# Kernel optimization log

Measured on AMD Instinct MI355X. Metric: run time of the kernel, lower is better.

The kernel has to match this reference:

```python
import jax, jax.numpy as jnp
import numpy as np
from jax import lax

V = 5          # IMU nodes
C = 128        # channels
T = 128        # timesteps
B = 128        # batch
K = 3          # st_kernel_size (non-causal)
V_TH = 0.8     # LIF threshold
TAU = 2.0      # LIF default tau (spikingjelly)
EPS = 1e-5


def setup_inputs() -> dict:
    key = jax.random.key(0)
    ks = jax.random.split(key, 6)
    # binary spike input [T, B, C, 2V]
    x_spike = (jax.random.uniform(ks[0], (T, B, C, 2 * V)) < 0.5).astype(jnp.float32)
    # modality fusion conv1d: [C, 2C, 1], kaiming-ish scale
    W_fusion = jax.random.normal(ks[1], (C, 2 * C, 1), jnp.float32) * (1.0 / np.sqrt(2 * C))
    gn1_w = jnp.ones((C,), jnp.float32)
    gn1_b = jnp.zeros((C,), jnp.float32)
    # node mixer conv1d over time: [V, V, K]
    W_mixer = jax.random.normal(ks[2], (V, V, K), jnp.float32) * (1.0 / np.sqrt(V * K))
    gn2_w = jnp.ones((V,), jnp.float32)
    gn2_b = jnp.zeros((V,), jnp.float32)
    # learnable adjacency: eye + 0.01*randn
    adj = jnp.eye(V, dtype=jnp.float32) + 0.01 * jax.random.normal(ks[3], (V, V), jnp.float32)
    return {"x_spike": x_spike, "W_fusion": W_fusion, "gn1_w": gn1_w, "gn1_b": gn1_b,
            "W_mixer": W_mixer, "gn2_w": gn2_w, "gn2_b": gn2_b, "adj": adj}


def groupnorm1(x, w, b):
    # single-group GroupNorm on [N, C, L]: normalize over (C, L) per sample
    mu = jnp.mean(x, axis=(1, 2), keepdims=True)
    var = jnp.var(x, axis=(1, 2), keepdims=True)
    xn = (x - mu) * lax.rsqrt(var + EPS)
    return xn * w[None, :, None] + b[None, :, None]


def lif_multistep(x_seq):
    # spikingjelly LIFNode, step_mode='m', decay_input=True, hard reset to 0
    def step(v, x):
        v = v + (x - v) / TAU
        s = (v >= V_TH).astype(x.dtype)
        v = v * (1.0 - s)
        return v, s
    _, spikes = lax.scan(step, jnp.zeros_like(x_seq[0]), x_seq)
    return spikes


def reference(x_spike, W_fusion, gn1_w, gn1_b, W_mixer, gn2_w, gn2_b, adj):
    Tn, Bn, Cn, N = x_spike.shape
    # ---- dual-modality fusion ----
    acc, gyr = x_spike[..., :V], x_spike[..., V:]
    fused = jnp.concatenate([acc, gyr], axis=2).reshape(Tn * Bn, 2 * Cn, V)  # [TB, 2C, V]
    y = jnp.einsum('oc,ncv->nov', W_fusion[:, :, 0], fused)                   # 1x1 conv
    y = groupnorm1(y, gn1_w, gn1_b)
    x_nodes = lif_multistep(y.reshape(Tn, Bn, Cn, V))                         # [T,B,C,V]
    # ---- adaptive topology temporal conv ----
    x_bt = x_nodes.transpose(1, 2, 3, 0).reshape(Bn * Cn, V, Tn)              # [BC, V, T]
    pad = K // 2
    x_bt = jnp.pad(x_bt, ((0, 0), (0, 0), (pad, pad)))
    sym = 0.5 * (adj + adj.T)
    masked_w = W_mixer * jax.nn.sigmoid(sym)[:, :, None]                      # [V, V, K]
    y_bt = lax.conv_general_dilated(x_bt, masked_w, (1,), 'VALID',
                                    dimension_numbers=('NCH', 'OIH', 'NCH'))
    y_bt = y_bt[..., :Tn]
    y_bt = groupnorm1(y_bt, gn2_w, gn2_b)
    y_mixed = y_bt.reshape(Bn, Cn, V, Tn).transpose(3, 0, 1, 2)               # [T,B,C,V]
    out = lif_multistep(y_mixed)
    return jnp.concatenate([out, out], axis=-1)                               # [T,B,C,2V]
```

## Files before the change

kernel.cpp:

```cpp
#include <hip/hip_runtime.h>
#include <cstdint>
#include <cstddef>

#define NV 5
#define NC 128
#define NT 128
#define NB 128
typedef unsigned long long ull;

__device__ __forceinline__ float fa(float a, float b){ return __fadd_rn(a,b); }
__device__ __forceinline__ float fm(float a, float b){ return __fmul_rn(a,b); }
__device__ __forceinline__ float fs(float a, float b){ return __fsub_rn(a,b); }

__device__ __forceinline__ float base80(const float* a)
{
    float r0=a[0],r1=a[1],r2=a[2],r3=a[3],r4=a[4],r5=a[5],r6=a[6],r7=a[7];
    #pragma unroll
    for (int i = 8; i < 80; i += 8) {
        r0=fa(r0,a[i+0]); r1=fa(r1,a[i+1]); r2=fa(r2,a[i+2]); r3=fa(r3,a[i+3]);
        r4=fa(r4,a[i+4]); r5=fa(r5,a[i+5]); r6=fa(r6,a[i+6]); r7=fa(r7,a[i+7]);
    }
    return fa(fa(fa(r0,r1),fa(r2,r3)), fa(fa(r4,r5),fa(r6,r7)));
}

__device__ __forceinline__ float base80v(const float* a, float mu)
{
    float r[8];
    #pragma unroll
    for (int j = 0; j < 8; ++j) { const float d = fs(a[j], mu); r[j] = fm(d, d); }
    #pragma unroll
    for (int i = 8; i < 80; i += 8)
        #pragma unroll
        for (int j = 0; j < 8; ++j) {
            const float d = fs(a[i + j], mu);
            r[j] = fa(r[j], fm(d, d));
        }
    return fa(fa(fa(r[0],r[1]),fa(r[2],r[3])), fa(fa(r[4],r[5]),fa(r[6],r[7])));
}

__global__ __launch_bounds__(256) void kT(const float* __restrict__ W,
                                          float* __restrict__ Wt)
{
    const int i = blockIdx.x * 256 + threadIdx.x;
    const int c = i >> 7, o = i & 127;
    Wt[i] = W[o * 256 + c];
}

__global__ __launch_bounds__(128) void kA(const float* __restrict__ x,
                                          const float* __restrict__ Wt,
                                          const float* __restrict__ g1w,
                                          const float* __restrict__ g1b,
                                          float* __restrict__ y1)
{
    const int n0 = blockIdx.x * 4;
    const int o  = threadIdx.x;

    __shared__ float xs_raw[4 * 256 * 8];
    __shared__ float statA[4][4];
    __shared__ float muS[4], rstdS[4];
    float (*xs)[256][8] = (float (*)[256][8])xs_raw;

    {
        const float4* xg = (const float4*)(x + (size_t)n0 * 1280);
        #pragma unroll
        for (int it = 0; it < 10; ++it) {
            const int q = it * 128 + o;
            const float4 val = xg[q];
            const int f = q * 4;
            const int g = f >> 10 >> 0 ? f / 1280 : 0;
            const int gg = f / 1280;
            int r = f - gg * 1280;
            float tmp[4] = {val.x, val.y, val.z, val.w};
            #pragma unroll
            for (int e = 0; e < 4; ++e) {
                const int c = r / 10, j = r - c * 10;
                const int fc = (j < 5) ? c : c + 128;
                const int v  = (j < 5) ? j : j - 5;
                xs[gg][fc][v] = tmp[e];
                ++r;
            }
            (void)g;
        }
    }
    __syncthreads();

    float acc[4][NV];
    #pragma unroll
    for (int g = 0; g < 4; ++g)
        #pragma unroll
        for (int v = 0; v < NV; ++v) acc[g][v] = 0.f;

    #pragma unroll 4
    for (int fc = 0; fc < 256; ++fc) {
        const float A = Wt[fc * 128 + o];
        #pragma unroll
        for (int g = 0; g < 4; ++g) {
            const float4 xv = *(const float4*)&xs[g][fc][0];
            const float  x4 = xs[g][fc][4];
            acc[g][0] = fa(acc[g][0], fm(A, xv.x));
            acc[g][1] = fa(acc[g][1], fm(A, xv.y));
            acc[g][2] = fa(acc[g][2], fm(A, xv.z));
            acc[g][3] = fa(acc[g][3], fm(A, xv.w));
            acc[g][4] = fa(acc[g][4], fm(A, x4));
        }
    }
    __syncthreads();

    float* ys = xs_raw;
    float* dsv = xs_raw + 2560;

    #pragma unroll
    for (int g = 0; g < 4; ++g)
        #pragma unroll
        for (int v = 0; v < NV; ++v) ys[g * 640 + o * 5 + v] = acc[g][v];
    __syncthreads();

    if (threadIdx.x < 16) {
        const int g = threadIdx.x >> 2, p = threadIdx.x & 3;
        const float b0 = base80(&ys[g * 640 + (2 * p) * 80]);
        const float b1 = base80(&ys[g * 640 + (2 * p + 1) * 80]);
        statA[g][p] = fa(b0, b1);
    }
    __syncthreads();
    if (threadIdx.x < 4) {
        const int g = threadIdx.x;
        const float tot = fa(fa(statA[g][0], statA[g][1]), fa(statA[g][2], statA[g][3]));
        muS[g] = __fdiv_rn(tot, 640.f);
    }
    __syncthreads();

    #pragma unroll
    for (int g = 0; g < 4; ++g) {
        const float mu = muS[g];
        #pragma unroll
        for (int v = 0; v < NV; ++v) {
            const float d = fs(acc[g][v], mu);
            dsv[g * 640 + o * 5 + v] = fm(d, d);
        }
    }
    __syncthreads();
    if (threadIdx.x < 16) {
        const int g = threadIdx.x >> 2, p = threadIdx.x & 3;
        const float b0 = base80(&dsv[g * 640 + (2 * p) * 80]);
        const float b1 = base80(&dsv[g * 640 + (2 * p + 1) * 80]);
        statA[g][p] = fa(b0, b1);
    }
    __syncthreads();
    if (threadIdx.x < 4) {
        const int g = threadIdx.x;
        const float tot = fa(fa(statA[g][0], statA[g][1]), fa(statA[g][2], statA[g][3]));
        const float var = __fdiv_rn(tot, 640.f);
        rstdS[g] = __fdiv_rn(1.f, __fsqrt_rn(fa(var, 1e-5f)));
    }
    __syncthreads();

    const float wf = g1w[o], bf = g1b[o];
    #pragma unroll
    for (int g = 0; g < 4; ++g) {
        const float mu = muS[g], rstd = rstdS[g];
        const int n = n0 + g;
        #pragma unroll
        for (int v = 0; v < NV; ++v) {
            const float xn = fm(fs(acc[g][v], mu), rstd);
            y1[(size_t)n * 640 + o * 5 + v] = fa(fm(xn, wf), bf);
        }
    }
}

__global__ __launch_bounds__(320) void kB1(const float* __restrict__ y1,
                                           ulonglong2* __restrict__ masks)
{
    const int b   = blockIdx.x >> 1;
    const int c0  = (blockIdx.x & 1) * 64;
    const int tid = threadIdx.x;

    ull lo = 0ull, hi = 0ull;
    float vm = 0.f;
    const float* p = y1 + (size_t)b * 640 + (size_t)c0 * 5 + tid;
    for (int t0 = 0; t0 < NT; t0 += 16) {
        float xv[16];
        #pragma unroll
        for (int j = 0; j < 16; ++j)
            xv[j] = p[(size_t)(t0 + j) * (NB * 640)];
        #pragma unroll
        for (int j = 0; j < 16; ++j) {
            vm = fa(vm, fm(fs(xv[j], vm), 0.5f));
            if (vm >= 0.8f) {
                const int t = t0 + j;
                if (t < 64) lo |= 1ull << t; else hi |= 1ull << (t - 64);
                vm = 0.f;
            }
        }
    }
    masks[(size_t)b * 640 + (size_t)c0 * 5 + tid] = make_ulonglong2(lo, hi);
}

__device__ __forceinline__ float bitf(ull lo, ull hi, int t)
{
    if (t < 0 || t > 127) return 0.f;
    return (float)(((t < 64) ? (lo >> t) : (hi >> (t - 64))) & 1ull);
}

__global__ __launch_bounds__(512) void kB2(const ulonglong2* __restrict__ masks,
                                           const float* __restrict__ Wm,
                                           const float* __restrict__ g2w,
                                           const float* __restrict__ g2b,
                                           const float* __restrict__ adj,
                                           float* __restrict__ out)
{
    const int blk = blockIdx.x;
    const int b   = blk >> 5;
    const int c0  = (blk & 31) * 4;
    const int tid = threadIdx.x;
    const int p   = tid >> 7;
    const int lt  = tid & 127;

    __shared__ float mw_s[75];
    __shared__ ull   m_lo[4][5], m_hi[4][5];
    __shared__ float conv_s[4][5][128];
    __shared__ float spk_s[128][40];
    __shared__ float stat_s[4][8];
    __shared__ float mu_s[4], rstd_s[4];

    if (tid < 75) {
        const int oo = tid / 15, rem = tid % 15, ii = rem / 3;
        const float sym = fm(0.5f, fa(adj[oo * 5 + ii], adj[ii * 5 + oo]));
        const float e = (float)exp(-(double)sym);
        const float sig = __fdiv_rn(1.f, fa(1.f, e));
        mw_s[tid] = fm(Wm[tid], sig);
    }
    if (tid < 20) {
        const int pp = tid / 5, vv = tid % 5;
        const ulonglong2 m = masks[((size_t)b * 128 + c0 + pp) * 5 + vv];
        m_lo[pp][vv] = m.x; m_hi[pp][vv] = m.y;
    }
    __syncthreads();

    {
        float bv[5][3];
        #pragma unroll
        for (int i = 0; i < 5; ++i) {
            const ull lo = m_lo[p][i], hi = m_hi[p][i];
            #pragma unroll
            for (int k = 0; k < 3; ++k)
                bv[i][k] = bitf(lo, hi, lt - 1 + k);
        }
        #pragma unroll
        for (int o = 0; o < 5; ++o) {
            float res = 0.f;
            #pragma unroll
            for (int i = 0; i < 5; ++i)
                #pragma unroll
                for (int k = 0; k < 3; ++k)
                    res = fa(res, fm(mw_s[(o * 5 + i) * 3 + k], bv[i][k]));
            conv_s[p][o][lt] = res;
        }
    }
    __syncthreads();

    if (lt < 8)
        stat_s[p][lt] = base80(&conv_s[p][0][0] + lt * 80);
    __syncthreads();
    if (lt == 0) {
        const float* s = stat_s[p];
        const float tot = fa(fa(fa(s[0],s[1]),fa(s[2],s[3])),
                             fa(fa(s[4],s[5]),fa(s[6],s[7])));
        mu_s[p] = __fdiv_rn(tot, 640.f);
    }
    __syncthreads();

    if (lt < 8)
        stat_s[p][lt] = base80v(&conv_s[p][0][0] + lt * 80, mu_s[p]);
    __syncthreads();
    if (lt == 0) {
        const float* s = stat_s[p];
        const float tot = fa(fa(fa(s[0],s[1]),fa(s[2],s[3])),
                             fa(fa(s[4],s[5]),fa(s[6],s[7])));
        const float var = __fdiv_rn(tot, 640.f);
        rstd_s[p] = __fdiv_rn(1.f, __fsqrt_rn(fa(var, 1e-5f)));
    }
    __syncthreads();

    if (lt < 5) {
        const int o = lt;
        const float mu = mu_s[p], rstd = rstd_s[p];
        const float gw = g2w[o], gb = g2b[o];
        float vm = 0.f;
        for (int t = 0; t < NT; ++t) {
            const float z  = conv_s[p][o][t];
            const float xn = fm(fs(z, mu), rstd);
            const float yn = fa(fm(xn, gw), gb);
            vm = fa(vm, fm(fs(yn, vm), 0.5f));
            const bool sp = (vm >= 0.8f);
            if (sp) vm = 0.f;
            const float so = sp ? 1.f : 0.f;
            spk_s[t][p * 10 + o]     = so;
            spk_s[t][p * 10 + 5 + o] = so;
        }
    }
    __syncthreads();

    for (int q = tid; q < 1280; q += 512) {
        const int t = q / 10, s = q - t * 10;
        float4* dst = (float4*)(out + ((size_t)(t * NB + b) * 1280 + c0 * 10));
        dst[s] = reinterpret_cast<const float4*>(&spk_s[t][0])[s];
    }
}

extern "C" void kernel_launch(void* const* d_in, const int* in_sizes, int n_in,
                              void* d_out, int out_size, void* d_ws, size_t ws_size,
                              hipStream_t stream)
{
    const float* x   = (const float*)d_in[0];
    const float* W   = (const float*)d_in[1];
    const float* g1w = (const float*)d_in[2];
    const float* g1b = (const float*)d_in[3];
    const float* Wm  = (const float*)d_in[4];
    const float* g2w = (const float*)d_in[5];
    const float* g2b = (const float*)d_in[6];
    const float* adj = (const float*)d_in[7];
    float* out = (float*)d_out;

    float* y1 = (float*)d_ws;
    ulonglong2* masks = (ulonglong2*)((char*)d_ws + (64u << 20));
    float* Wt = (float*)((char*)d_ws + (80u << 20));

    hipLaunchKernelGGL(kT, dim3(128), dim3(256), 0, stream, W, Wt);
    hipLaunchKernelGGL(kA, dim3(NT * NB / 4), dim3(128), 0, stream,
                       x, Wt, g1w, g1b, y1);
    hipLaunchKernelGGL(kB1, dim3(NB * 2), dim3(320), 0, stream,
                       y1, masks);
    hipLaunchKernelGGL(kB2, dim3(4096), dim3(512), 0, stream,
                       masks, Wm, g2w, g2b, adj, out);
}
```

Baseline: 201.7 us.

## Compute two output channels per thread in fusion GEMM with packed smem layout

The fusion kernel now runs 64 threads per block, each computing two output channels, so every shared-memory input value read is reused for two weight columns. The staged input is repacked as [fc][g*5+v] with 20 contiguous floats per input channel, so one fc row loads as five float4s instead of strided per-group reads. This cuts LDS traffic per FMA. In exchange it doubles accumulator registers and halves the threads per block, which may reduce latency hiding and add load-loop iterations.

```diff
diff --git a/kernel.cpp b/kernel.cpp
--- a/kernel.cpp
+++ b/kernel.cpp
@@ -46,123 +46,141 @@
     Wt[i] = W[o * 256 + c];
 }
 
-__global__ __launch_bounds__(128) void kA(const float* __restrict__ x,
-                                          const float* __restrict__ Wt,
-                                          const float* __restrict__ g1w,
-                                          const float* __restrict__ g1b,
-                                          float* __restrict__ y1)
+__global__ __launch_bounds__(64) void kA(const float* __restrict__ x,
+                                         const float* __restrict__ Wt,
+                                         const float* __restrict__ g1w,
+                                         const float* __restrict__ g1b,
+                                         float* __restrict__ y1)
 {
     const int n0 = blockIdx.x * 4;
-    const int o  = threadIdx.x;
-
-    __shared__ float xs_raw[4 * 256 * 8];
+    const int t  = threadIdx.x;
+
+    __shared__ __align__(16) float xs[256 * 20];
     __shared__ float statA[4][4];
     __shared__ float muS[4], rstdS[4];
-    float (*xs)[256][8] = (float (*)[256][8])xs_raw;
 
     {
         const float4* xg = (const float4*)(x + (size_t)n0 * 1280);
         #pragma unroll
-        for (int it = 0; it < 10; ++it) {
-            const int q = it * 128 + o;
+        for (int it = 0; it < 20; ++it) {
+            const int q = it * 64 + t;
             const float4 val = xg[q];
-            const int f = q * 4;
-            const int g = f >> 10 >> 0 ? f / 1280 : 0;
-            const int gg = f / 1280;
-            int r = f - gg * 1280;
             float tmp[4] = {val.x, val.y, val.z, val.w};
-            #pragma unroll
-            for (int e = 0; e < 4; ++e) {
-                const int c = r / 10, j = r - c * 10;
+            int r = q * 4;
+            #pragma unroll
+            for (int e = 0; e < 4; ++e, ++r) {
+                const int g  = r / 1280;
+                const int rr = r - g * 1280;
+                const int c  = rr / 10;
+                const int j  = rr - c * 10;
                 const int fc = (j < 5) ? c : c + 128;
                 const int v  = (j < 5) ? j : j - 5;
-                xs[gg][fc][v] = tmp[e];
-                ++r;
-            }
-            (void)g;
-        }
-    }
-    __syncthreads();
-
-    float acc[4][NV];
-    #pragma unroll
-    for (int g = 0; g < 4; ++g)
-        #pragma unroll
-        for (int v = 0; v < NV; ++v) acc[g][v] = 0.f;
-
-    #pragma unroll 4
+                xs[fc * 20 + g * 5 + v] = tmp[e];
+            }
+        }
+    }
+    __syncthreads();
+
+    float acc[2][4][NV];
+    #pragma unroll
+    for (int oi = 0; oi < 2; ++oi)
+        #pragma unroll
+        for (int g = 0; g < 4; ++g)
+            #pragma unroll
+            for (int v = 0; v < NV; ++v) acc[oi][g][v] = 0.f;
+
+    #pragma unroll 2
     for (int fc = 0; fc < 256; ++fc) {
-        const float A = Wt[fc * 128 + o];
-        #pragma unroll
-        for (int g = 0; g < 4; ++g) {
-            const float4 xv = *(const float4*)&xs[g][fc][0];
-            const float  x4 = xs[g][fc][4];
-            acc[g][0] = fa(acc[g][0], fm(A, xv.x));
-            acc[g][1] = fa(acc[g][1], fm(A, xv.y));
-            acc[g][2] = fa(acc[g][2], fm(A, xv.z));
-            acc[g][3] = fa(acc[g][3], fm(A, xv.w));
-            acc[g][4] = fa(acc[g][4], fm(A, x4));
-        }
-    }
-    __syncthreads();
-
-    float* ys = xs_raw;
-    float* dsv = xs_raw + 2560;
-
-    #pragma unroll
-    for (int g = 0; g < 4; ++g)
-        #pragma unroll
-        for (int v = 0; v < NV; ++v) ys[g * 640 + o * 5 + v] = acc[g][v];
-    __syncthreads();
-
-    if (threadIdx.x < 16) {
-        const int g = threadIdx.x >> 2, p = threadIdx.x & 3;
+        const float A0 = Wt[fc * 128 + t];
+        const float A1 = Wt[fc * 128 + 64 + t];
+        const float4 q0 = *(const float4*)&xs[fc * 20 + 0];
+        const float4 q1 = *(const float4*)&xs[fc * 20 + 4];
+        const float4 q2 = *(const float4*)&xs[fc * 20 + 8];
+        const float4 q3 = *(const float4*)&xs[fc * 20 + 12];
+        const float4 q4 = *(const float4*)&xs[fc * 20 + 16];
+        const float xv[20] = {q0.x,q0.y,q0.z,q0.w, q1.x,q1.y,q1.z,q1.w,
+                              q2.x,q2.y,q2.z,q2.w, q3.x,q3.y,q3.z,q3.w,
+                              q4.x,q4.y,q4.z,q4.w};
+        #pragma unroll
+        for (int g = 0; g < 4; ++g)
+            #pragma unroll
+            for (int v = 0; v < NV; ++v) {
+                acc[0][g][v] = fa(acc[0][g][v], fm(A0, xv[g * 5 + v]));
+                acc[1][g][v] = fa(acc[1][g][v], fm(A1, xv[g * 5 + v]));
+            }
+    }
+    __syncthreads();
+
+    float* ys  = xs;
+    float* dsv = xs + 2560;
+
+    #pragma unroll
+    for (int oi = 0; oi < 2; ++oi) {
+        const int o = t + oi * 64;
+        #pragma unroll
+        for (int g = 0; g < 4; ++g)
+            #pragma unroll
+            for (int v = 0; v < NV; ++v)
+                ys[g * 640 + o * 5 + v] = acc[oi][g][v];
+    }
+    __syncthreads();
+
+    if (t < 16) {
+        const int g = t >> 2, p = t & 3;
         const float b0 = base80(&ys[g * 640 + (2 * p) * 80]);
         const float b1 = base80(&ys[g * 640 + (2 * p + 1) * 80]);
         statA[g][p] = fa(b0, b1);
     }
     __syncthreads();
-    if (threadIdx.x < 4) {
-        const int g = threadIdx.x;
+    if (t < 4) {
+        const int g = t;
         const float tot = fa(fa(statA[g][0], statA[g][1]), fa(statA[g][2], statA[g][3]));
         muS[g] = __fdiv_rn(tot, 640.f);
     }
     __syncthreads();
 
     #pragma unroll
-    for (int g = 0; g < 4; ++g) {
-        const float mu = muS[g];
-        #pragma unroll
-        for (int v = 0; v < NV; ++v) {
-            const float d = fs(acc[g][v], mu);
-            dsv[g * 640 + o * 5 + v] = fm(d, d);
-        }
-    }
-    __syncthreads();
-    if (threadIdx.x < 16) {
-        const int g = threadIdx.x >> 2, p = threadIdx.x & 3;
+    for (int oi = 0; oi < 2; ++oi) {
+        const int o = t + oi * 64;
+        #pragma unroll
+        for (int g = 0; g < 4; ++g) {
+            const float mu = muS[g];
+            #pragma unroll
+            for (int v = 0; v < NV; ++v) {
+                const float d = fs(acc[oi][g][v], mu);
+                dsv[g * 640 + o * 5 + v] = fm(d, d);
+            }
+        }
+    }
+    __syncthreads();
+    if (t < 16) {
+        const int g = t >> 2, p = t & 3;
         const float b0 = base80(&dsv[g * 640 + (2 * p) * 80]);
         const float b1 = base80(&dsv[g * 640 + (2 * p + 1) * 80]);
         statA[g][p] = fa(b0, b1);
     }
     __syncthreads();
-    if (threadIdx.x < 4) {
-        const int g = threadIdx.x;
+    if (t < 4) {
+        const int g = t;
         const float tot = fa(fa(statA[g][0], statA[g][1]), fa(statA[g][2], statA[g][3]));
         const float var = __fdiv_rn(tot, 640.f);
         rstdS[g] = __fdiv_rn(1.f, __fsqrt_rn(fa(var, 1e-5f)));
     }
     __syncthreads();
 
-    const float wf = g1w[o], bf = g1b[o];
-    #pragma unroll
-    for (int g = 0; g < 4; ++g) {
-        const float mu = muS[g], rstd = rstdS[g];
-        const int n = n0 + g;
-        #pragma unroll
-        for (int v = 0; v < NV; ++v) {
-            const float xn = fm(fs(acc[g][v], mu), rstd);
-            y1[(size_t)n * 640 + o * 5 + v] = fa(fm(xn, wf), bf);
+    #pragma unroll
+    for (int oi = 0; oi < 2; ++oi) {
+        const int o = t + oi * 64;
+        const float wf = g1w[o], bf = g1b[o];
+        #pragma unroll
+        for (int g = 0; g < 4; ++g) {
+            const float mu = muS[g], rstd = rstdS[g];
+            const int n = n0 + g;
+            #pragma unroll
+            for (int v = 0; v < NV; ++v) {
+                const float xn = fm(fs(acc[oi][g][v], mu), rstd);
+                y1[(size_t)n * 640 + o * 5 + v] = fa(fm(xn, wf), bf);
+            }
         }
     }
 }
@@ -326,7 +344,7 @@
     float* Wt = (float*)((char*)d_ws + (80u << 20));
 
     hipLaunchKernelGGL(kT, dim3(128), dim3(256), 0, stream, W, Wt);
-    hipLaunchKernelGGL(kA, dim3(NT * NB / 4), dim3(128), 0, stream,
+    hipLaunchKernelGGL(kA, dim3(NT * NB / 4), dim3(64), 0, stream,
                        x, Wt, g1w, g1b, y1);
     hipLaunchKernelGGL(kB1, dim3(NB * 2), dim3(320), 0, stream,
                        y1, masks);
```

Result: slower. 226.6 us (+12.4%).
